# Kernel tuning notes

Hardware: AMD Instinct MI355X
Metric: run time of the kernel (lower is better)

## Reference

```python
import jax, jax.numpy as jnp
import numpy as np

D_MODEL = 2048
D_INNER = 2048
D_XB = 512
D_STATE = 32
DT_RANK = 128
D_FF = 5632
BATCH = 2
SEQ = 1024
EPS = 1e-5


def _rmsnorm(x, w):
    var = jnp.mean(jnp.square(x), axis=-1, keepdims=True)
    return x * jax.lax.rsqrt(var + EPS) * w


def _selective_scan(x, dt, A, B, C):
    # x, dt: [b,l,g,p]; A: [g,p,n]; B, C: [b,l,g,n]  (p == n == D_STATE here)
    b, l, g, p = x.shape
    n = A.shape[-1]

    def step(h, inp):
        x_t, dt_t, B_t, C_t = inp                                  # [b,g,p],[b,g,p],[b,g,n],[b,g,n]
        dA = jnp.exp(dt_t[..., None] * A)                          # [b,g,p,n]
        h = dA * h + (dt_t * x_t)[..., None] * B_t[:, :, None, :]  # ZOH discretization
        y = jnp.einsum('bgpn,bgn->bgp', h, C_t)
        return h, y

    h0 = jnp.zeros((b, g, p, n), x.dtype)
    xs = tuple(jnp.moveaxis(a, 1, 0) for a in (x, dt, B, C))       # time-major
    _, ys = jax.lax.scan(step, h0, xs)
    return jnp.moveaxis(ys, 0, 1)                                  # [b,l,g,p]


def _mamba(u, in_proj_w, dt_proj_w, dt_proj_b, A_log, D_param, out_proj_w):
    b, l, _ = u.shape
    zxbcdt = u @ in_proj_w.T                                       # [b,l,2*d_inner+2*d_xb+dt_rank]
    splits = np.cumsum([D_INNER, D_XB, D_XB, D_INNER]).tolist()
    z, x, Bc, Cc, dt_raw = jnp.split(zxbcdt, splits, axis=-1)
    dt = jax.nn.softplus(dt_raw @ dt_proj_w.T + dt_proj_b)         # [b,l,d_inner]

    g = D_INNER // D_STATE        # 64 heads (Q/V side)
    g_kv = D_XB // D_STATE        # 16 kv groups
    rep = g // g_kv
    x = jnp.repeat(x.reshape(b, l, g_kv, D_STATE), rep, axis=2)    # V -> x, [b,l,g,p]
    Bm = jnp.repeat(Bc.reshape(b, l, g_kv, D_STATE), rep, axis=2)  # K -> B, [b,l,g,n]
    Cm = Cc.reshape(b, l, g, D_STATE)                              # Q -> C, [b,l,g,n]
    A = -jnp.exp(A_log).reshape(g, D_STATE, D_STATE)               # [g,p,n]
    dt = dt.reshape(b, l, g, D_STATE)

    y = _selective_scan(x, dt, A, Bm, Cm).reshape(b, l, D_INNER)
    y = y + x.reshape(b, l, D_INNER) * D_param                     # skip term D*x
    y = y * jax.nn.silu(z)                                         # gate
    return y @ out_proj_w.T


def _forward(hidden_states, in_proj_w, dt_proj_w, dt_proj_b, A_log, D_param,
             out_proj_w, gate_w, up_w, down_w, norm1_w, norm2_w):
    h = hidden_states + _mamba(_rmsnorm(hidden_states, norm1_w), in_proj_w,
                               dt_proj_w, dt_proj_b, A_log, D_param, out_proj_w)
    xn = _rmsnorm(h, norm2_w)
    mlp = (jax.nn.silu(xn @ gate_w.T) * (xn @ up_w.T)) @ down_w.T
    return h + mlp


def setup_inputs() -> dict:
    key = jax.random.key(0)
    ks = jax.random.split(key, 8)
    s = lambda k, shape, scale=0.02: jax.random.normal(k, shape, jnp.float32) * scale
    proj_dim = 2 * D_INNER + 2 * D_XB + DT_RANK
    return {
        'hidden_states': jax.random.normal(ks[0], (BATCH, SEQ, D_MODEL), jnp.float32),
        'in_proj_w': s(ks[1], (proj_dim, D_MODEL)),
        'dt_proj_w': s(ks[2], (D_INNER, DT_RANK)),
        'dt_proj_b': jnp.full((D_INNER,), -4.6, jnp.float32),  # softplus -> dt ~ 0.01
        'A_log': jnp.log(jnp.tile(jnp.arange(1, D_STATE + 1, dtype=jnp.float32), (D_INNER, 1))),
        'D_param': jnp.ones((D_INNER,), jnp.float32),
        'out_proj_w': s(ks[3], (D_MODEL, D_INNER)),
        'gate_w': s(ks[4], (D_FF, D_MODEL)),
        'up_w': s(ks[5], (D_FF, D_MODEL)),
        'down_w': s(ks[6], (D_MODEL, D_FF)),
        'norm1_w': jnp.ones((D_MODEL,), jnp.float32),
        'norm2_w': jnp.ones((D_MODEL,), jnp.float32),
    }


def reference(hidden_states, in_proj_w, dt_proj_w, dt_proj_b, A_log, D_param,
              out_proj_w, gate_w, up_w, down_w, norm1_w, norm2_w):
    return _forward(hidden_states, in_proj_w, dt_proj_w, dt_proj_b, A_log, D_param,
                    out_proj_w, gate_w, up_w, down_w, norm1_w, norm2_w)
```

## Files before the change

### kernel.cpp

```cpp
#include <hip/hip_runtime.h>


typedef __attribute__((ext_vector_type(4))) float f32x4;
typedef __attribute__((ext_vector_type(8))) __bf16 bf16x8;

#define NC 16
#define TC 64

__device__ __forceinline__ unsigned short f2b(float f) {
  unsigned u = __builtin_bit_cast(unsigned, f);
  u += 0x7fffu + ((u >> 16) & 1u);
  return (unsigned short)(u >> 16);
}
__device__ __forceinline__ float b2f(unsigned short b) {
  return __builtin_bit_cast(float, ((unsigned)b) << 16);
}

__global__ __launch_bounds__(256) void cvt_bf16(const float2* __restrict__ in,
                                                unsigned int* __restrict__ out,
                                                int n2) {
  int i = blockIdx.x * 256 + threadIdx.x;
  if (i >= n2) return;
  float2 v = in[i];
  out[i] = (unsigned)f2b(v.x) | ((unsigned)f2b(v.y) << 16);
}

__global__ __launch_bounds__(256) void rmsnorm_cast(const float* __restrict__ x,
                                                    const float* __restrict__ w,
                                                    unsigned short* __restrict__ out) {
  int row = blockIdx.x;
  int t = threadIdx.x;
  const float* xr = x + (size_t)row * 2048;
  float4 v0 = *(const float4*)&xr[t * 8];
  float4 v1 = *(const float4*)&xr[t * 8 + 4];
  float s = v0.x * v0.x + v0.y * v0.y + v0.z * v0.z + v0.w * v0.w +
            v1.x * v1.x + v1.y * v1.y + v1.z * v1.z + v1.w * v1.w;
#pragma unroll
  for (int off = 1; off < 64; off <<= 1) s += __shfl_xor(s, off);
  __shared__ float red[4];
  if ((t & 63) == 0) red[t >> 6] = s;
  __syncthreads();
  s = red[0] + red[1] + red[2] + red[3];
  float scale = rsqrtf(s * (1.0f / 2048.0f) + 1e-5f);
  float4 w0 = *(const float4*)&w[t * 8];
  float4 w1 = *(const float4*)&w[t * 8 + 4];
  uint4 o;
  o.x = (unsigned)f2b(v0.x * scale * w0.x) | ((unsigned)f2b(v0.y * scale * w0.y) << 16);
  o.y = (unsigned)f2b(v0.z * scale * w0.z) | ((unsigned)f2b(v0.w * scale * w0.w) << 16);
  o.z = (unsigned)f2b(v1.x * scale * w1.x) | ((unsigned)f2b(v1.y * scale * w1.y) << 16);
  o.w = (unsigned)f2b(v1.z * scale * w1.z) | ((unsigned)f2b(v1.w * scale * w1.w) << 16);
  *(uint4*)&out[(size_t)row * 2048 + t * 8] = o;
}

__global__ __launch_bounds__(256) void cast_dtraw(const float* __restrict__ zx,
                                                  unsigned short* __restrict__ dst) {
  int i = blockIdx.x * 256 + threadIdx.x;
  int r = i >> 7, c = i & 127;
  dst[i] = f2b(zx[(size_t)r * 5248 + 5120 + c]);
}

template <int EPI>
__global__ __launch_bounds__(256, 2) void gemm_bt(
    const unsigned short* __restrict__ A, const unsigned short* __restrict__ B,
    float* __restrict__ outf, unsigned short* __restrict__ outb,
    const float* __restrict__ auxf, const unsigned short* __restrict__ auxb,
    int N, int K) {
  __shared__ unsigned short As[128 * 64];
  __shared__ unsigned short Bs[128 * 64];
  const int tid = threadIdx.x;
  const int l = tid & 63;
  const int wid = tid >> 6;
  const int m0 = blockIdx.y * 128, n0 = blockIdx.x * 128;
  const int wr = wid >> 1, wc = wid & 1;

  f32x4 zero = {0.f, 0.f, 0.f, 0.f};
  f32x4 acc[4][4];
#pragma unroll
  for (int i = 0; i < 4; ++i)
#pragma unroll
    for (int j = 0; j < 4; ++j) acc[i][j] = zero;

  const int rlock = l >> 3;
  const int clog = (l & 7) ^ rlock;

  for (int kt = 0; kt < K; kt += 64) {
#pragma unroll
    for (int j = 0; j < 4; ++j) {
      int chunk = wid * 4 + j;
      int row = chunk * 8 + rlock;
      const unsigned short* ga = A + (size_t)(m0 + row) * K + kt + clog * 8;
      __builtin_amdgcn_global_load_lds(
          (const __attribute__((address_space(1))) void*)ga,
          (__attribute__((address_space(3))) void*)(As + chunk * 512), 16, 0, 0);
      const unsigned short* gb = B + (size_t)(n0 + row) * K + kt + clog * 8;
      __builtin_amdgcn_global_load_lds(
          (const __attribute__((address_space(1))) void*)gb,
          (__attribute__((address_space(3))) void*)(Bs + chunk * 512), 16, 0, 0);
    }
    asm volatile("s_waitcnt vmcnt(0)" ::: "memory");
    __syncthreads();

#pragma unroll
    for (int ks = 0; ks < 2; ++ks) {
      bf16x8 af[4], bfr[4];
#pragma unroll
      for (int mi = 0; mi < 4; ++mi) {
        int row = wr * 64 + mi * 16 + (l & 15);
        int c = ks * 4 + (l >> 4);
        int phys = c ^ (row & 7);
        af[mi] = *(const bf16x8*)&As[row * 64 + phys * 8];
      }
#pragma unroll
      for (int ni = 0; ni < 4; ++ni) {
        int row = wc * 64 + ni * 16 + (l & 15);
        int c = ks * 4 + (l >> 4);
        int phys = c ^ (row & 7);
        bfr[ni] = *(const bf16x8*)&Bs[row * 64 + phys * 8];
      }
#pragma unroll
      for (int mi = 0; mi < 4; ++mi)
#pragma unroll
        for (int ni = 0; ni < 4; ++ni)
          acc[mi][ni] = __builtin_amdgcn_mfma_f32_16x16x32_bf16(
              af[mi], bfr[ni], acc[mi][ni], 0, 0, 0);
    }
    __syncthreads();
  }

#pragma unroll
  for (int mi = 0; mi < 4; ++mi) {
#pragma unroll
    for (int ni = 0; ni < 4; ++ni) {
#pragma unroll
      for (int r = 0; r < 4; ++r) {
        int row = m0 + wr * 64 + mi * 16 + (l >> 4) * 4 + r;
        int col = n0 + wc * 64 + ni * 16 + (l & 15);
        size_t idx = (size_t)row * N + col;
        float v = acc[mi][ni][r];
        if constexpr (EPI == 0) {
          outf[idx] = v;
        } else if constexpr (EPI == 1) {
          float x = v + auxf[col];
          outf[idx] = (x > 15.f) ? x : __logf(1.f + __expf(x));
        } else if constexpr (EPI == 2) {
          outf[idx] = v + auxf[idx];
        } else if constexpr (EPI == 3) {
          outb[idx] = f2b(v);
        } else {
          float gv = b2f(auxb[idx]);
          float sg = gv / (1.f + __expf(-gv));
          outb[idx] = f2b(sg * v);
        }
      }
    }
  }
}

__global__ __launch_bounds__(256) void scan_partial(
    const float* __restrict__ zx, const float* __restrict__ dtb,
    const float* __restrict__ A_log,
    float* __restrict__ hpart, float* __restrict__ aprod) {
  int lane = threadIdx.x & 63;
  int w = blockIdx.x * 4 + (threadIdx.x >> 6);
  int chunk = w & (NC - 1);
  int gh = w >> 4;
  int b = gh >> 7;
  int rem = gh & 127;
  int g = rem >> 1;
  int ph = rem & 1;
  int p_loc = lane >> 2;
  int ngrp = lane & 3;
  int p = ph * 16 + p_loc;
  int n0 = ngrp * 8;
  int gp = g * 32 + p;

  float4 a0 = *(const float4*)&A_log[(size_t)gp * 32 + n0];
  float4 a1 = *(const float4*)&A_log[(size_t)gp * 32 + n0 + 4];
  float Ar[8] = {-__expf(a0.x), -__expf(a0.y), -__expf(a0.z), -__expf(a0.w),
                 -__expf(a1.x), -__expf(a1.y), -__expf(a1.z), -__expf(a1.w)};

  const float* prow = zx + (size_t)(b * 1024 + chunk * TC) * 5248;
  const float* pdt = dtb + (size_t)(b * 1024 + chunk * TC) * 2048 + gp;
  const int xoff = 2048 + (g >> 2) * 32 + p;
  const int boff = 2560 + (g >> 2) * 32 + n0;

  float h[8];
#pragma unroll
  for (int j = 0; j < 8; ++j) h[j] = 0.f;
  float S = 0.f;

#pragma unroll 2
  for (int t = 0; t < TC; ++t) {
    float dtv = *pdt;
    float xv = prow[xoff];
    float4 B0 = *(const float4*)&prow[boff];
    float4 B1 = *(const float4*)&prow[boff + 4];
    float dtx = dtv * xv;
    S += dtv;
    float Bv[8] = {B0.x, B0.y, B0.z, B0.w, B1.x, B1.y, B1.z, B1.w};
#pragma unroll
    for (int j = 0; j < 8; ++j) {
      float dA = __expf(dtv * Ar[j]);
      h[j] = fmaf(dA, h[j], dtx * Bv[j]);
    }
    prow += 5248;
    pdt += 2048;
  }

  size_t e0 = (size_t)chunk * 131072 + (size_t)b * 65536 + (size_t)gp * 32 + n0;
  float4 h0 = {h[0], h[1], h[2], h[3]};
  float4 h1 = {h[4], h[5], h[6], h[7]};
  *(float4*)&hpart[e0] = h0;
  *(float4*)&hpart[e0 + 4] = h1;
  float4 p0 = {__expf(Ar[0] * S), __expf(Ar[1] * S), __expf(Ar[2] * S), __expf(Ar[3] * S)};
  float4 p1 = {__expf(Ar[4] * S), __expf(Ar[5] * S), __expf(Ar[6] * S), __expf(Ar[7] * S)};
  *(float4*)&aprod[e0] = p0;
  *(float4*)&aprod[e0 + 4] = p1;
}

__global__ __launch_bounds__(256) void scan_combine(
    const float* __restrict__ hpart, const float* __restrict__ aprod,
    float* __restrict__ H0) {
  int e = blockIdx.x * 256 + threadIdx.x;
  float H = 0.f;
#pragma unroll
  for (int c = 0; c < NC; ++c) {
    H0[(size_t)c * 131072 + e] = H;
    H = fmaf(aprod[(size_t)c * 131072 + e], H, hpart[(size_t)c * 131072 + e]);
  }
}

__global__ __launch_bounds__(256) void scan_final(
    const float* __restrict__ zx, const float* __restrict__ dtb,
    const float* __restrict__ A_log, const float* __restrict__ D_param,
    const float* __restrict__ H0, unsigned short* __restrict__ ygated) {
  int lane = threadIdx.x & 63;
  int w = blockIdx.x * 4 + (threadIdx.x >> 6);
  int chunk = w & (NC - 1);
  int gh = w >> 4;
  int b = gh >> 7;
  int rem = gh & 127;
  int g = rem >> 1;
  int ph = rem & 1;
  int p_loc = lane >> 2;
  int ngrp = lane & 3;
  int p = ph * 16 + p_loc;
  int n0 = ngrp * 8;
  int gp = g * 32 + p;

  float4 a0 = *(const float4*)&A_log[(size_t)gp * 32 + n0];
  float4 a1 = *(const float4*)&A_log[(size_t)gp * 32 + n0 + 4];
  float Ar[8] = {-__expf(a0.x), -__expf(a0.y), -__expf(a0.z), -__expf(a0.w),
                 -__expf(a1.x), -__expf(a1.y), -__expf(a1.z), -__expf(a1.w)};
  float Dv = D_param[gp];

  const float* prow = zx + (size_t)(b * 1024 + chunk * TC) * 5248;
  const float* pdt = dtb + (size_t)(b * 1024 + chunk * TC) * 2048 + gp;
  unsigned short* py = ygated + (size_t)(b * 1024 + chunk * TC) * 2048 + gp;
  const int xoff = 2048 + (g >> 2) * 32 + p;
  const int boff = 2560 + (g >> 2) * 32 + n0;
  const int coff = 3072 + g * 32 + n0;

  size_t e0 = (size_t)chunk * 131072 + (size_t)b * 65536 + (size_t)gp * 32 + n0;
  float4 h04 = *(const float4*)&H0[e0];
  float4 h14 = *(const float4*)&H0[e0 + 4];
  float h[8] = {h04.x, h04.y, h04.z, h04.w, h14.x, h14.y, h14.z, h14.w};

#pragma unroll 2
  for (int t = 0; t < TC; ++t) {
    float dtv = *pdt;
    float xv = prow[xoff];
    float4 B0 = *(const float4*)&prow[boff];
    float4 B1 = *(const float4*)&prow[boff + 4];
    float4 C0 = *(const float4*)&prow[coff];
    float4 C1 = *(const float4*)&prow[coff + 4];
    float dtx = dtv * xv;
    float Bv[8] = {B0.x, B0.y, B0.z, B0.w, B1.x, B1.y, B1.z, B1.w};
    float Cv[8] = {C0.x, C0.y, C0.z, C0.w, C1.x, C1.y, C1.z, C1.w};
    float y0 = 0.f, y1 = 0.f;
#pragma unroll
    for (int j = 0; j < 8; ++j) {
      float dA = __expf(dtv * Ar[j]);
      h[j] = fmaf(dA, h[j], dtx * Bv[j]);
      if (j & 1) y1 = fmaf(h[j], Cv[j], y1);
      else       y0 = fmaf(h[j], Cv[j], y0);
    }
    float yc = y0 + y1;
    yc += __shfl_xor(yc, 1);
    yc += __shfl_xor(yc, 2);
    if (ngrp == 0) {
      float y = fmaf(xv, Dv, yc);
      float zv = prow[gp];
      float sg = zv / (1.f + __expf(-zv));
      *py = f2b(y * sg);
    }
    prow += 5248;
    pdt += 2048;
    py += 2048;
  }
}

extern "C" void kernel_launch(void* const* d_in, const int* in_sizes, int n_in,
                              void* d_out, int out_size, void* d_ws, size_t ws_size,
                              hipStream_t stream) {
  const float* hidden    = (const float*)d_in[0];
  const float* in_proj_w = (const float*)d_in[1];
  const float* dt_proj_w = (const float*)d_in[2];
  const float* dt_proj_b = (const float*)d_in[3];
  const float* A_log     = (const float*)d_in[4];
  const float* D_param   = (const float*)d_in[5];
  const float* out_proj_w= (const float*)d_in[6];
  const float* gate_w    = (const float*)d_in[7];
  const float* up_w      = (const float*)d_in[8];
  const float* down_w    = (const float*)d_in[9];
  const float* norm1_w   = (const float*)d_in[10];
  const float* norm2_w   = (const float*)d_in[11];
  float* out = (float*)d_out;
  char* ws = (char*)d_ws;

  const size_t o_w_in   = 0;
  const size_t o_w_dt   = 21495808;
  const size_t o_w_out  = 22020096;
  const size_t o_w_gate = 30408704;
  const size_t o_w_up   = 53477376;
  const size_t o_w_down = 76546048;
  const size_t o_u      = 99614720;
  const size_t o_zx     = 108003328;
  const size_t o_dtraw  = 150994944;
  const size_t o_dtbuf  = 151519232;
  const size_t o_yg     = 168296448;
  const size_t o_h      = 176685056;

  unsigned short* w_in   = (unsigned short*)(ws + o_w_in);
  unsigned short* w_dt   = (unsigned short*)(ws + o_w_dt);
  unsigned short* w_out  = (unsigned short*)(ws + o_w_out);
  unsigned short* w_gate = (unsigned short*)(ws + o_w_gate);
  unsigned short* w_up   = (unsigned short*)(ws + o_w_up);
  unsigned short* w_down = (unsigned short*)(ws + o_w_down);
  unsigned short* u_bf   = (unsigned short*)(ws + o_u);
  unsigned short* xn_bf  = (unsigned short*)(ws + o_u);
  float*          zxb    = (float*)(ws + o_zx);
  unsigned short* gate_b = (unsigned short*)(ws + o_zx);
  unsigned short* dtraw  = (unsigned short*)(ws + o_dtraw);
  float*          dtbuf  = (float*)(ws + o_dtbuf);
  unsigned short* hsig   = (unsigned short*)(ws + o_dtbuf);
  unsigned short* yg     = (unsigned short*)(ws + o_yg);
  float*          hbuf   = (float*)(ws + o_h);
  float* hpart = (float*)(ws + o_h);
  float* aprod = (float*)(ws + o_h + 8388608);
  float* H0buf = (float*)(ws + o_u);

  auto cvt = [&](const float* src, unsigned short* dst, size_t n) {
    int n2 = (int)(n / 2);
    cvt_bf16<<<(n2 + 255) / 256, 256, 0, stream>>>((const float2*)src,
                                                   (unsigned int*)dst, n2);
  };

  cvt(in_proj_w, w_in, (size_t)5248 * 2048);
  cvt(dt_proj_w, w_dt, (size_t)2048 * 128);
  cvt(out_proj_w, w_out, (size_t)2048 * 2048);
  cvt(gate_w, w_gate, (size_t)5632 * 2048);
  cvt(up_w, w_up, (size_t)5632 * 2048);
  cvt(down_w, w_down, (size_t)2048 * 5632);

  rmsnorm_cast<<<2048, 256, 0, stream>>>(hidden, norm1_w, u_bf);

  gemm_bt<0><<<dim3(5248 / 128, 16), 256, 0, stream>>>(
      u_bf, w_in, zxb, nullptr, nullptr, nullptr, 5248, 2048);

  cast_dtraw<<<1024, 256, 0, stream>>>(zxb, dtraw);

  gemm_bt<1><<<dim3(16, 16), 256, 0, stream>>>(
      dtraw, w_dt, dtbuf, nullptr, dt_proj_b, nullptr, 2048, 128);

  scan_partial<<<1024, 256, 0, stream>>>(zxb, dtbuf, A_log, hpart, aprod);
  scan_combine<<<512, 256, 0, stream>>>(hpart, aprod, H0buf);
  scan_final<<<1024, 256, 0, stream>>>(zxb, dtbuf, A_log, D_param, H0buf, yg);

  gemm_bt<2><<<dim3(16, 16), 256, 0, stream>>>(
      yg, w_out, hbuf, nullptr, hidden, nullptr, 2048, 2048);

  rmsnorm_cast<<<2048, 256, 0, stream>>>(hbuf, norm2_w, xn_bf);

  gemm_bt<3><<<dim3(5632 / 128, 16), 256, 0, stream>>>(
      xn_bf, w_gate, nullptr, gate_b, nullptr, nullptr, 5632, 2048);

  gemm_bt<4><<<dim3(5632 / 128, 16), 256, 0, stream>>>(
      xn_bf, w_up, nullptr, hsig, nullptr, gate_b, 5632, 2048);

  gemm_bt<2><<<dim3(16, 16), 256, 0, stream>>>(
      hsig, w_down, out, nullptr, hbuf, nullptr, 2048, 5632);
}
```

Before: 668.2 us.

## Split-K the out-proj and down-proj GEMMs with atomic accumulation

Adds a K-split parameter to the GEMM kernel and runs the two 2048x2048-output GEMMs (out_proj and down_proj) with four K-chunks on a third grid axis. Partial results are accumulated into the output with atomic adds, after the residual is first copied into the output buffer. Only 256 tiles covered the 256 CUs before, so this is meant to raise occupancy and parallelism. The cost is atomic traffic, two extra copy kernels, and a summation order that is no longer deterministic.

```diff
diff --git a/kernel.cpp b/kernel.cpp
--- a/kernel.cpp
+++ b/kernel.cpp
@@ -23,6 +23,12 @@
   if (i >= n2) return;
   float2 v = in[i];
   out[i] = (unsigned)f2b(v.x) | ((unsigned)f2b(v.y) << 16);
+}
+
+__global__ __launch_bounds__(256) void copy_f32(const float4* __restrict__ in,
+                                                float4* __restrict__ out, int n4) {
+  int i = blockIdx.x * 256 + threadIdx.x;
+  if (i < n4) out[i] = in[i];
 }
 
 __global__ __launch_bounds__(256) void rmsnorm_cast(const float* __restrict__ x,
@@ -64,7 +70,7 @@
     const unsigned short* __restrict__ A, const unsigned short* __restrict__ B,
     float* __restrict__ outf, unsigned short* __restrict__ outb,
     const float* __restrict__ auxf, const unsigned short* __restrict__ auxb,
-    int N, int K) {
+    int N, int K, int Kchunk) {
   __shared__ unsigned short As[128 * 64];
   __shared__ unsigned short Bs[128 * 64];
   const int tid = threadIdx.x;
@@ -83,7 +89,8 @@
   const int rlock = l >> 3;
   const int clog = (l & 7) ^ rlock;
 
-  for (int kt = 0; kt < K; kt += 64) {
+  const int kt0 = blockIdx.z * Kchunk;
+  for (int kt = kt0; kt < kt0 + Kchunk; kt += 64) {
 #pragma unroll
     for (int j = 0; j < 4; ++j) {
       int chunk = wid * 4 + j;
@@ -146,10 +153,12 @@
           outf[idx] = v + auxf[idx];
         } else if constexpr (EPI == 3) {
           outb[idx] = f2b(v);
-        } else {
+        } else if constexpr (EPI == 4) {
           float gv = b2f(auxb[idx]);
           float sg = gv / (1.f + __expf(-gv));
           outb[idx] = f2b(sg * v);
+        } else {
+          unsafeAtomicAdd(&outf[idx], v);
         }
       }
     }
@@ -366,28 +375,32 @@
   rmsnorm_cast<<<2048, 256, 0, stream>>>(hidden, norm1_w, u_bf);
 
   gemm_bt<0><<<dim3(5248 / 128, 16), 256, 0, stream>>>(
-      u_bf, w_in, zxb, nullptr, nullptr, nullptr, 5248, 2048);
+      u_bf, w_in, zxb, nullptr, nullptr, nullptr, 5248, 2048, 2048);
 
   cast_dtraw<<<1024, 256, 0, stream>>>(zxb, dtraw);
 
   gemm_bt<1><<<dim3(16, 16), 256, 0, stream>>>(
-      dtraw, w_dt, dtbuf, nullptr, dt_proj_b, nullptr, 2048, 128);
+      dtraw, w_dt, dtbuf, nullptr, dt_proj_b, nullptr, 2048, 128, 128);
 
   scan_partial<<<1024, 256, 0, stream>>>(zxb, dtbuf, A_log, hpart, aprod);
   scan_combine<<<512, 256, 0, stream>>>(hpart, aprod, H0buf);
   scan_final<<<1024, 256, 0, stream>>>(zxb, dtbuf, A_log, D_param, H0buf, yg);
 
-  gemm_bt<2><<<dim3(16, 16), 256, 0, stream>>>(
-      yg, w_out, hbuf, nullptr, hidden, nullptr, 2048, 2048);
+  copy_f32<<<4096, 256, 0, stream>>>((const float4*)hidden, (float4*)hbuf,
+                                     1048576);
+  gemm_bt<5><<<dim3(16, 16, 4), 256, 0, stream>>>(
+      yg, w_out, hbuf, nullptr, nullptr, nullptr, 2048, 2048, 512);
 
   rmsnorm_cast<<<2048, 256, 0, stream>>>(hbuf, norm2_w, xn_bf);
 
   gemm_bt<3><<<dim3(5632 / 128, 16), 256, 0, stream>>>(
-      xn_bf, w_gate, nullptr, gate_b, nullptr, nullptr, 5632, 2048);
+      xn_bf, w_gate, nullptr, gate_b, nullptr, nullptr, 5632, 2048, 2048);
 
   gemm_bt<4><<<dim3(5632 / 128, 16), 256, 0, stream>>>(
-      xn_bf, w_up, nullptr, hsig, nullptr, gate_b, 5632, 2048);
-
-  gemm_bt<2><<<dim3(16, 16), 256, 0, stream>>>(
-      hsig, w_down, out, nullptr, hbuf, nullptr, 2048, 5632);
-}
+      xn_bf, w_up, nullptr, hsig, nullptr, gate_b, 5632, 2048, 2048);
+
+  copy_f32<<<4096, 256, 0, stream>>>((const float4*)hbuf, (float4*)out,
+                                     1048576);
+  gemm_bt<5><<<dim3(16, 16, 4), 256, 0, stream>>>(
+      hsig, w_down, out, nullptr, nullptr, nullptr, 2048, 5632, 1408);
+}
```

After: 688.1 us. 3.0% more time.
